# Performance work log

Hardware: AMD Instinct MI355X
Metric: run time of the kernel (lower is better)

## Reference

```python
import jax, jax.numpy as jnp
import numpy as np
import math

N_NODES = 50000
N_EDGES = 800000
IN_FEATS = 128
HID = 64
OUT = 2
D = 2  # num_layers


def calc_thetas(d):
    """Beta-distribution polynomial coefficients (ascending order), matching
    sympy.poly((x/2)**i * (1-x/2)**(d-i) / Beta(i+1, d+1-i)) with inverted coeffs."""
    thetas = []
    for i in range(d + 1):
        p1 = np.zeros(i + 1)
        p1[-1] = 0.5 ** i  # (x/2)^i, ascending coeffs
        p2 = np.array([math.comb(d - i, j) * (-0.5) ** j for j in range(d - i + 1)])  # (1-x/2)^(d-i)
        beta = math.factorial(i) * math.factorial(d - i) / math.factorial(d + 1)
        thetas.append((np.convolve(p1, p2) / beta).tolist())
    return thetas


def poly_branch(h, src, dst, thetas):
    """Run all PolyConv filters on activated features h; concat along feature dim."""
    n = h.shape[0]
    deg = jnp.zeros((n,), h.dtype).at[dst].add(jnp.ones((dst.shape[0],), h.dtype))
    dinv = jnp.clip(deg, 1.0, None) ** -0.5  # D^{-1/2} of in-degrees, clamped min 1
    dinv = dinv[:, None]
    outs = []
    for th in thetas:
        f = h
        acc = th[0] * h
        for k in range(1, len(th)):
            # feat <- feat - D^{-1/2} A D^{-1/2} feat  (copy_u / sum aggregation)
            agg = jax.ops.segment_sum((f * dinv)[src], dst, num_segments=n)
            f = f - agg * dinv
            acc = acc + th[k] * f
        outs.append(acc)
    return jnp.concatenate(outs, axis=-1)


def setup_inputs() -> dict:
    key = jax.random.key(0)
    ks = jax.random.split(key, 12)
    inp = {
        "x": jax.random.normal(ks[0], (N_NODES, IN_FEATS), jnp.float32),
        "sim_x": jax.random.normal(ks[1], (N_NODES, IN_FEATS), jnp.float32),
        "src": jax.random.randint(ks[2], (N_EDGES,), 0, N_NODES, jnp.int32),
        "dst": jax.random.randint(ks[3], (N_EDGES,), 0, N_NODES, jnp.int32),
        "sim_src": jax.random.randint(ks[4], (N_EDGES,), 0, N_NODES, jnp.int32),
        "sim_dst": jax.random.randint(ks[5], (N_EDGES,), 0, N_NODES, jnp.int32),
        "W1_o": jax.random.normal(ks[6], (IN_FEATS, HID), jnp.float32) / np.sqrt(IN_FEATS),
        "b1_o": jnp.zeros((HID,), jnp.float32),
        "W1_s": jax.random.normal(ks[7], (IN_FEATS, HID), jnp.float32) / np.sqrt(IN_FEATS),
        "b1_s": jnp.zeros((HID,), jnp.float32),
        "Wm1": jax.random.normal(ks[8], (HID * (D + 1) * 2, HID), jnp.float32) / np.sqrt(HID * (D + 1) * 2),
        "bm1": jnp.zeros((HID,), jnp.float32),
        "Wm2": jax.random.normal(ks[9], (HID, OUT), jnp.float32) / np.sqrt(HID),
        "bm2": jnp.zeros((OUT,), jnp.float32),
    }
    return inp


def reference(x, sim_x, src, dst, sim_src, sim_dst,
              W1_o, b1_o, W1_s, b1_s, Wm1, bm1, Wm2, bm2):
    thetas_o = calc_thetas(D)
    thetas_s = [[4.0] * (D + 1) for _ in range(D + 1)]  # conv_s uses constant theta=4

    h = jax.nn.relu(x @ W1_o + b1_o)
    h_final = poly_branch(h, src, dst, thetas_o)      # [N, HID*(D+1)]

    sh = jax.nn.relu(sim_x @ W1_s + b1_s)
    sim_h_final = poly_branch(sh, sim_src, sim_dst, thetas_s)

    h_all = jnp.concatenate([h_final, sim_h_final], axis=-1)  # [N, HID*(D+1)*2]
    logits = jax.nn.relu(h_all @ Wm1 + bm1) @ Wm2 + bm2
    return (h_all, logits)
```

## Files before the change

### kernel.cpp

```cpp
#include <hip/hip_runtime.h>
#include <hip/hip_fp16.h>
#include <hip/hip_fp8.h>


#define KB_BITS 10
#define KMAX 64
#define PCHUNK 4096
#define PVPT 16
#define PADMAX 7168

__device__ __forceinline__ float cv8(unsigned char b) {
    __hip_fp8_e4m3 v; v.__x = b; return (float)v;
}
__device__ __forceinline__ unsigned char to8(float f) {
    __hip_fp8_e4m3 v(f); return v.__x;
}

__global__ __launch_bounds__(256) void bhist_kernel(
    const int* __restrict__ dst, const int* __restrict__ sim_dst,
    int* __restrict__ bhist, int E, int Es) {
    __shared__ int h[2 * KMAX];
    int tid = threadIdx.x;
    if (tid < 2 * KMAX) h[tid] = 0;
    __syncthreads();
    int total = E + Es;
    for (int e = blockIdx.x * 256 + tid; e < total; e += gridDim.x * 256) {
        if (e < E) atomicAdd(&h[dst[e] >> KB_BITS], 1);
        else       atomicAdd(&h[KMAX + (sim_dst[e - E] >> KB_BITS)], 1);
    }
    __syncthreads();
    if (tid < 2 * KMAX && h[tid]) atomicAdd(&bhist[tid], h[tid]);
}

__global__ __launch_bounds__(128) void bscan_kernel(
    const int* __restrict__ bhist, int* __restrict__ brow,
    int* __restrict__ gcur) {
    int g = threadIdx.x >> 6, lane = threadIdx.x & 63;
    int v = bhist[g * KMAX + lane];
    int inc = v;
    #pragma unroll
    for (int off = 1; off < 64; off <<= 1) {
        int u = __shfl_up(inc, off);
        if (lane >= off) inc += u;
    }
    int ex = inc - v;
    brow[g * (KMAX + 1) + lane] = ex;
    if (lane == 63) brow[g * (KMAX + 1) + KMAX] = inc;
    gcur[g * KMAX + lane] = ex;
}

__global__ __launch_bounds__(256) void partition_kernel(
    const int* __restrict__ src, const int* __restrict__ dst,
    const int* __restrict__ sim_src, const int* __restrict__ sim_dst,
    int* __restrict__ gcur, unsigned* __restrict__ staged,
    int E, int Es, int nbo) {
    int b = blockIdx.x;
    const int* S; const int* D; int Eg; int goff; unsigned* stg;
    if (b < nbo) { S = src; D = dst; Eg = E; goff = 0; stg = staged; }
    else { b -= nbo; S = sim_src; D = sim_dst; Eg = Es; goff = KMAX; stg = staged + E; }
    int e0 = b * PCHUNK;
    int cnt_blk = Eg - e0; if (cnt_blk > PCHUNK) cnt_blk = PCHUNK;
    __shared__ int hist[KMAX], basep[KMAX], cur[KMAX], gbase[KMAX];
    __shared__ unsigned srt[PCHUNK];
    int tid = threadIdx.x;
    if (tid < KMAX) hist[tid] = 0;
    __syncthreads();
    unsigned full[PVPT];
    #pragma unroll
    for (int i = 0; i < PVPT; ++i) {
        int idx = i * 256 + tid;
        if (idx < cnt_blk) {
            int e = e0 + idx;
            int d = D[e];
            unsigned bk = (unsigned)d >> KB_BITS;
            full[i] = (bk << 26) | ((unsigned)S[e] << KB_BITS) |
                      (unsigned)(d & ((1 << KB_BITS) - 1));
            atomicAdd(&hist[bk], 1);
        } else full[i] = 0xFFFFFFFFu;
    }
    __syncthreads();
    if (tid < 64) {
        int v = hist[tid];
        int inc = v;
        #pragma unroll
        for (int off = 1; off < 64; off <<= 1) {
            int u = __shfl_up(inc, off);
            if (tid >= off) inc += u;
        }
        int ex = inc - v;
        basep[tid] = ex;
        cur[tid] = ex;
        gbase[tid] = v ? atomicAdd(&gcur[goff + tid], v) : 0;
    }
    __syncthreads();
    #pragma unroll
    for (int i = 0; i < PVPT; ++i) {
        unsigned f = full[i];
        if (f != 0xFFFFFFFFu) {
            unsigned bk = f >> 26;
            int slot = atomicAdd(&cur[bk], 1);
            srt[slot] = f;
        }
    }
    __syncthreads();
    for (int slot = tid; slot < cnt_blk; slot += 256) {
        unsigned f = srt[slot];
        unsigned bk = f >> 26;
        int gpos = gbase[bk] + (slot - basep[bk]);
        stg[gpos] = f & 0x3FFFFFFu;
    }
}

__global__ __launch_bounds__(512) void place_kernel(
    const unsigned* __restrict__ staged, const int* __restrict__ brow,
    int* __restrict__ row_o, int* __restrict__ row_s,
    int* __restrict__ pend_o, int* __restrict__ pend_s,
    unsigned short* __restrict__ esrc_o, unsigned short* __restrict__ esrc_s,
    float* __restrict__ dinv, int N, int K, int E, int pad) {
    int b = blockIdx.x;
    const unsigned* stg; const int* br; int* row; int* pend;
    unsigned short* esrc; float* dv;
    if (b < K) { stg = staged; br = brow; row = row_o; pend = pend_o; esrc = esrc_o; dv = dinv; }
    else { b -= K; stg = staged + E; br = brow + (KMAX + 1); row = row_s; pend = pend_s; esrc = esrc_s; dv = dinv + N; }
    int node0 = b << KB_BITS;
    int nn = N - node0; if (nn > (1 << KB_BITS)) nn = (1 << KB_BITS);
    int seg0 = br[b], seg1 = br[b + 1];
    int base = pad ? (seg0 + b * PADMAX) : seg0;
    __shared__ int ncnt[1 << KB_BITS];
    __shared__ int wsum[8];
    int tid = threadIdx.x;
    for (int i = tid; i < (1 << KB_BITS); i += 512) ncnt[i] = 0;
    __syncthreads();
    for (int j = seg0 + tid; j < seg1; j += 512)
        atomicAdd(&ncnt[stg[j] & ((1 << KB_BITS) - 1)], 1);
    __syncthreads();
    int i0 = tid * 2;
    int v0 = ncnt[i0], v1 = ncnt[i0 + 1];
    int p0 = pad ? ((v0 + 7) & ~7) : v0;
    int p1 = pad ? ((v1 + 7) & ~7) : v1;
    int s = p0 + p1;
    int inc = s;
    #pragma unroll
    for (int off = 1; off < 64; off <<= 1) {
        int u = __shfl_up(inc, off);
        if ((tid & 63) >= off) inc += u;
    }
    if ((tid & 63) == 63) wsum[tid >> 6] = inc;
    __syncthreads();
    int wo = 0;
    for (int w = 0; w < (tid >> 6); ++w) wo += wsum[w];
    int ex = base + wo + inc - s;
    if (i0 < nn) {
        row[node0 + i0] = ex;
        pend[node0 + i0] = ex + p0;
        dv[node0 + i0] = rsqrtf((float)(v0 > 1 ? v0 : 1));
        for (int q = ex + v0; q < ex + p0; ++q) esrc[q] = (unsigned short)N;
    }
    if (i0 + 1 < nn) {
        int ex2 = ex + p0;
        row[node0 + i0 + 1] = ex2;
        pend[node0 + i0 + 1] = ex2 + p1;
        dv[node0 + i0 + 1] = rsqrtf((float)(v1 > 1 ? v1 : 1));
        for (int q = ex2 + v1; q < ex2 + p1; ++q) esrc[q] = (unsigned short)N;
    }
    if (!pad && b == K - 1 && tid == 0) row[N] = br[K];
    __syncthreads();
    ncnt[i0] = ex;
    ncnt[i0 + 1] = ex + p0;
    __syncthreads();
    for (int j = seg0 + tid; j < seg1; j += 512) {
        unsigned f = stg[j];
        int pos = atomicAdd(&ncnt[f & ((1 << KB_BITS) - 1)], 1);
        esrc[pos] = (unsigned short)(f >> KB_BITS);
    }
}

__global__ __launch_bounds__(256) void fold_kernel(
    const float* __restrict__ Wm1, float* __restrict__ w1f,
    int* __restrict__ bhist) {
    int i = blockIdx.x * 256 + threadIdx.x;
    if (blockIdx.x == 0 && threadIdx.x < 2 * KMAX) bhist[threadIdx.x] = 0;
    if (i >= 256 * 64) return;
    int k = i >> 6, j = i & 63;
    float v = Wm1[k * 64 + j];
    if (k >= 192) v += Wm1[(k + 64) * 64 + j] + Wm1[(k + 128) * 64 + j];
    w1f[i] = v;
}

__global__ __launch_bounds__(256) void in_gemm2_kernel(
    const float* __restrict__ x, const float* __restrict__ sim_x,
    const float* __restrict__ W1_o, const float* __restrict__ b1_o,
    const float* __restrict__ W1_s, const float* __restrict__ b1_s,
    float* __restrict__ hall, __half* __restrict__ h16_o, __half* __restrict__ h16_s,
    __half* __restrict__ g16_o, __half* __restrict__ g16_s,
    unsigned char* __restrict__ h8_o, unsigned char* __restrict__ h8_s,
    unsigned char* __restrict__ g8_o, unsigned char* __restrict__ g8_s,
    const float* __restrict__ dinv, int n, int nbh, int f16path, int pad, int use8) {
    int bb = blockIdx.x;
    const float* xin; const float* W; const float* b; __half* h16;
    unsigned char* h8; const float* dinvv; int off;
    if (bb < nbh) { xin = x; W = W1_o; b = b1_o; h16 = h16_o; h8 = h8_o; dinvv = dinv; off = 0; }
    else { bb -= nbh; xin = sim_x; W = W1_s; b = b1_s; h16 = h16_s; h8 = h8_s; dinvv = dinv + n; off = 192; }
    if (pad && threadIdx.x < 64) {
        if (blockIdx.x == 0) {
            h16_o[(long)n * 64 + threadIdx.x] = __float2half_rn(0.f);
            g16_o[(long)n * 64 + threadIdx.x] = __float2half_rn(0.f);
            if (use8) { h8_o[(long)n * 64 + threadIdx.x] = 0; g8_o[(long)n * 64 + threadIdx.x] = 0; }
        } else if (blockIdx.x == nbh) {
            h16_s[(long)n * 64 + threadIdx.x] = __float2half_rn(0.f);
            g16_s[(long)n * 64 + threadIdx.x] = __float2half_rn(0.f);
            if (use8) { h8_s[(long)n * 64 + threadIdx.x] = 0; g8_s[(long)n * 64 + threadIdx.x] = 0; }
        }
    }
    __shared__ float xs[64][132];
    __shared__ float Wf[128][68];
    int tid = threadIdx.x;
    int node0 = bb * 64;
    const float4* wsrc = (const float4*)W;
    for (int i = tid; i < 2048; i += 256)
        *(float4*)&Wf[i >> 4][(i & 15) * 4] = wsrc[i];
    const float4* xsrc = (const float4*)xin;
    for (int i = tid; i < 2048; i += 256) {
        int nl = i >> 5, c = i & 31;
        int node = node0 + nl;
        float4 v = make_float4(0.f, 0.f, 0.f, 0.f);
        if (node < n) v = xsrc[(long)node * 32 + c];
        *(float4*)&xs[nl][c * 4] = v;
    }
    __syncthreads();
    int tx = tid & 15, ty = tid >> 4;
    float acc[4][4] = {};
    #pragma unroll 2
    for (int k = 0; k < 128; k += 4) {
        float4 a[4], bbv[4];
        #pragma unroll
        for (int i = 0; i < 4; ++i) a[i] = *(const float4*)&xs[ty * 4 + i][k];
        #pragma unroll
        for (int j = 0; j < 4; ++j) bbv[j] = *(const float4*)&Wf[k + j][tx * 4];
        #pragma unroll
        for (int i = 0; i < 4; ++i) {
            acc[i][0] = fmaf(a[i].x, bbv[0].x, acc[i][0]);
            acc[i][1] = fmaf(a[i].x, bbv[0].y, acc[i][1]);
            acc[i][2] = fmaf(a[i].x, bbv[0].z, acc[i][2]);
            acc[i][3] = fmaf(a[i].x, bbv[0].w, acc[i][3]);
            acc[i][0] = fmaf(a[i].y, bbv[1].x, acc[i][0]);
            acc[i][1] = fmaf(a[i].y, bbv[1].y, acc[i][1]);
            acc[i][2] = fmaf(a[i].y, bbv[1].z, acc[i][2]);
            acc[i][3] = fmaf(a[i].y, bbv[1].w, acc[i][3]);
            acc[i][0] = fmaf(a[i].z, bbv[2].x, acc[i][0]);
            acc[i][1] = fmaf(a[i].z, bbv[2].y, acc[i][1]);
            acc[i][2] = fmaf(a[i].z, bbv[2].z, acc[i][2]);
            acc[i][3] = fmaf(a[i].z, bbv[2].w, acc[i][3]);
            acc[i][0] = fmaf(a[i].w, bbv[3].x, acc[i][0]);
            acc[i][1] = fmaf(a[i].w, bbv[3].y, acc[i][1]);
            acc[i][2] = fmaf(a[i].w, bbv[3].z, acc[i][2]);
            acc[i][3] = fmaf(a[i].w, bbv[3].w, acc[i][3]);
        }
    }
    float4 bias = *(const float4*)&b[tx * 4];
    #pragma unroll
    for (int i = 0; i < 4; ++i) {
        int node = node0 + ty * 4 + i;
        if (node >= n) break;
        float4 r;
        r.x = fmaxf(acc[i][0] + bias.x, 0.0f);
        r.y = fmaxf(acc[i][1] + bias.y, 0.0f);
        r.z = fmaxf(acc[i][2] + bias.z, 0.0f);
        r.w = fmaxf(acc[i][3] + bias.w, 0.0f);
        if (f16path) {
            float dvn = dinvv[node];
            float v0 = r.x * dvn, v1 = r.y * dvn, v2 = r.z * dvn, v3 = r.w * dvn;
            __half hh[4];
            hh[0] = __float2half_rn(v0);
            hh[1] = __float2half_rn(v1);
            hh[2] = __float2half_rn(v2);
            hh[3] = __float2half_rn(v3);
            *(float2*)&h16[(long)node * 64 + tx * 4] = *(float2*)hh;
            if (use8) {
                uchar4 q;
                q.x = to8(v0); q.y = to8(v1); q.z = to8(v2); q.w = to8(v3);
                *(uchar4*)&h8[(long)node * 64 + tx * 4] = q;
            }
        } else {
            *(float4*)&hall[(long)node * 384 + off + tx * 4] = r;
        }
    }
}

__global__ __launch_bounds__(256) void hop1_kernel(
    const int* __restrict__ row_o, const int* __restrict__ pend_o,
    const unsigned short* __restrict__ esrc_o, const float* __restrict__ dinv_o,
    const int* __restrict__ row_s, const int* __restrict__ pend_s,
    const unsigned short* __restrict__ esrc_s, const float* __restrict__ dinv_s,
    const __half* __restrict__ h16_o, const __half* __restrict__ h16_s,
    __half* __restrict__ g16_o, __half* __restrict__ g16_s,
    const unsigned char* __restrict__ h8_o, const unsigned char* __restrict__ h8_s,
    unsigned char* __restrict__ g8_o, unsigned char* __restrict__ g8_s,
    int n, int nb, int use8) {
    int b = blockIdx.x;
    const int* row; const int* pend; const unsigned short* esrc;
    const float* dinv; const __half* h16; __half* g16;
    const unsigned char* h8; unsigned char* g8;
    if (b < nb) { row = row_o; pend = pend_o; esrc = esrc_o; dinv = dinv_o;
                  h16 = h16_o; g16 = g16_o; h8 = h8_o; g8 = g8_o; }
    else { b -= nb; row = row_s; pend = pend_s; esrc = esrc_s; dinv = dinv_s;
           h16 = h16_s; g16 = g16_s; h8 = h8_s; g8 = g8_s; }
    int d = b * 4 + (threadIdx.x >> 6);
    if (d >= n) return;
    int lane = threadIdx.x & 63;
    int p = row[d], end = pend[d];
    float dd = dinv[d];
    float h16v = __half2float(h16[((unsigned)d << 6) | lane]);
    float a0 = 0.f, a1 = 0.f, a2 = 0.f, a3 = 0.f;
    if (use8) {
        for (; p + 16 <= end; p += 16) {
            unsigned ss[16];
            #pragma unroll
            for (int i = 0; i < 16; ++i) ss[i] = esrc[p + i];
            #pragma unroll
            for (int i = 0; i < 16; i += 4) {
                a0 += cv8(h8[(ss[i] << 6) | lane]);
                a1 += cv8(h8[(ss[i + 1] << 6) | lane]);
                a2 += cv8(h8[(ss[i + 2] << 6) | lane]);
                a3 += cv8(h8[(ss[i + 3] << 6) | lane]);
            }
        }
        if (p + 8 <= end) {
            unsigned ss[8];
            #pragma unroll
            for (int i = 0; i < 8; ++i) ss[i] = esrc[p + i];
            #pragma unroll
            for (int i = 0; i < 8; i += 4) {
                a0 += cv8(h8[(ss[i] << 6) | lane]);
                a1 += cv8(h8[(ss[i + 1] << 6) | lane]);
                a2 += cv8(h8[(ss[i + 2] << 6) | lane]);
                a3 += cv8(h8[(ss[i + 3] << 6) | lane]);
            }
            p += 8;
        }
        for (; p < end; ++p)
            a0 += cv8(h8[((unsigned)esrc[p] << 6) | lane]);
    } else {
        for (; p + 16 <= end; p += 16) {
            unsigned ss[16];
            #pragma unroll
            for (int i = 0; i < 16; ++i) ss[i] = esrc[p + i];
            #pragma unroll
            for (int i = 0; i < 16; i += 4) {
                a0 += __half2float(h16[(ss[i] << 6) | lane]);
                a1 += __half2float(h16[(ss[i + 1] << 6) | lane]);
                a2 += __half2float(h16[(ss[i + 2] << 6) | lane]);
                a3 += __half2float(h16[(ss[i + 3] << 6) | lane]);
            }
        }
        if (p + 8 <= end) {
            unsigned ss[8];
            #pragma unroll
            for (int i = 0; i < 8; ++i) ss[i] = esrc[p + i];
            #pragma unroll
            for (int i = 0; i < 8; i += 4) {
                a0 += __half2float(h16[(ss[i] << 6) | lane]);
                a1 += __half2float(h16[(ss[i + 1] << 6) | lane]);
                a2 += __half2float(h16[(ss[i + 2] << 6) | lane]);
                a3 += __half2float(h16[(ss[i + 3] << 6) | lane]);
            }
            p += 8;
        }
        for (; p + 4 <= end; p += 4) {
            unsigned s0 = esrc[p], s1 = esrc[p + 1], s2 = esrc[p + 2], s3 = esrc[p + 3];
            a0 += __half2float(h16[(s0 << 6) | lane]);
            a1 += __half2float(h16[(s1 << 6) | lane]);
            a2 += __half2float(h16[(s2 << 6) | lane]);
            a3 += __half2float(h16[(s3 << 6) | lane]);
        }
        for (; p < end; ++p)
            a0 += __half2float(h16[((unsigned)esrc[p] << 6) | lane]);
    }
    float acc = (a0 + a1) + (a2 + a3);
    float val = h16v - acc * dd * dd;
    g16[((unsigned)d << 6) | lane] = __float2half_rn(val);
    if (use8) g8[((unsigned)d << 6) | lane] = to8(val);
}

__global__ __launch_bounds__(256) void hop2_kernel(
    const int* __restrict__ row_o, const int* __restrict__ pend_o,
    const unsigned short* __restrict__ esrc_o, const float* __restrict__ dinv_o,
    const int* __restrict__ row_s, const int* __restrict__ pend_s,
    const unsigned short* __restrict__ esrc_s, const float* __restrict__ dinv_s,
    const __half* __restrict__ h16_o, const __half* __restrict__ h16_s,
    const __half* __restrict__ g16_o, const __half* __restrict__ g16_s,
    const unsigned char* __restrict__ g8_o, const unsigned char* __restrict__ g8_s,
    float* __restrict__ hall, int n, int nb, int use8) {
    int b = blockIdx.x;
    int g = (b < nb) ? 0 : 1;
    const int* row; const int* pend; const unsigned short* esrc;
    const float* dinv; const __half* h16; const __half* g16;
    const unsigned char* g8;
    if (g == 0) { row = row_o; pend = pend_o; esrc = esrc_o; dinv = dinv_o;
                  h16 = h16_o; g16 = g16_o; g8 = g8_o; }
    else { b -= nb; row = row_s; pend = pend_s; esrc = esrc_s; dinv = dinv_s;
           h16 = h16_s; g16 = g16_s; g8 = g8_s; }
    int d = b * 4 + (threadIdx.x >> 6);
    if (d >= n) return;
    int lane = threadIdx.x & 63;
    int p = row[d], end = pend[d];
    float dd = dinv[d];
    float sq = 1.0f / dd;
    float f0 = __half2float(h16[((unsigned)d << 6) | lane]) * sq;
    float f1 = __half2float(g16[((unsigned)d << 6) | lane]) * sq;
    float a0 = 0.f, a1 = 0.f, a2 = 0.f, a3 = 0.f;
    if (use8) {
        for (; p + 16 <= end; p += 16) {
            unsigned ss[16];
            #pragma unroll
            for (int i = 0; i < 16; ++i) ss[i] = esrc[p + i];
            #pragma unroll
            for (int i = 0; i < 16; i += 4) {
                a0 += cv8(g8[(ss[i] << 6) | lane]);
                a1 += cv8(g8[(ss[i + 1] << 6) | lane]);
                a2 += cv8(g8[(ss[i + 2] << 6) | lane]);
                a3 += cv8(g8[(ss[i + 3] << 6) | lane]);
            }
        }
        if (p + 8 <= end) {
            unsigned ss[8];
            #pragma unroll
            for (int i = 0; i < 8; ++i) ss[i] = esrc[p + i];
            #pragma unroll
            for (int i = 0; i < 8; i += 4) {
                a0 += cv8(g8[(ss[i] << 6) | lane]);
                a1 += cv8(g8[(ss[i + 1] << 6) | lane]);
                a2 += cv8(g8[(ss[i + 2] << 6) | lane]);
                a3 += cv8(g8[(ss[i + 3] << 6) | lane]);
            }
            p += 8;
        }
        for (; p < end; ++p)
            a0 += cv8(g8[((unsigned)esrc[p] << 6) | lane]);
    } else {
        for (; p + 16 <= end; p += 16) {
            unsigned ss[16];
            #pragma unroll
            for (int i = 0; i < 16; ++i) ss[i] = esrc[p + i];
            #pragma unroll
            for (int i = 0; i < 16; i += 4) {
                a0 += __half2float(g16[(ss[i] << 6) | lane]);
                a1 += __half2float(g16[(ss[i + 1] << 6) | lane]);
                a2 += __half2float(g16[(ss[i + 2] << 6) | lane]);
                a3 += __half2float(g16[(ss[i + 3] << 6) | lane]);
            }
        }
        if (p + 8 <= end) {
            unsigned ss[8];
            #pragma unroll
            for (int i = 0; i < 8; ++i) ss[i] = esrc[p + i];
            #pragma unroll
            for (int i = 0; i < 8; i += 4) {
                a0 += __half2float(g16[(ss[i] << 6) | lane]);
                a1 += __half2float(g16[(ss[i + 1] << 6) | lane]);
                a2 += __half2float(g16[(ss[i + 2] << 6) | lane]);
                a3 += __half2float(g16[(ss[i + 3] << 6) | lane]);
            }
            p += 8;
        }
        for (; p + 4 <= end; p += 4) {
            unsigned s0 = esrc[p], s1 = esrc[p + 1], s2 = esrc[p + 2], s3 = esrc[p + 3];
            a0 += __half2float(g16[(s0 << 6) | lane]);
            a1 += __half2float(g16[(s1 << 6) | lane]);
            a2 += __half2float(g16[(s2 << 6) | lane]);
            a3 += __half2float(g16[(s3 << 6) | lane]);
        }
        for (; p < end; ++p)
            a0 += __half2float(g16[((unsigned)esrc[p] << 6) | lane]);
    }
    float acc = (a0 + a1) + (a2 + a3);
    float f2 = f1 - acc * dd;
    long ob = (long)d * 384 + lane;
    if (g == 0) {
        hall[ob]       = 3.0f * f0 - 3.0f * f1 + 0.75f * f2;
        hall[ob + 64]  = 3.0f * f1 - 1.5f * f2;
        hall[ob + 128] = 0.75f * f2;
    } else {
        float ss = 4.0f * (f0 + f1 + f2);
        hall[ob + 192] = ss; hall[ob + 256] = ss; hall[ob + 320] = ss;
    }
}

__global__ __launch_bounds__(256) void gather2_kernel(
    const int* __restrict__ row_o, const unsigned short* __restrict__ esrc_o,
    const float* __restrict__ dinv_o,
    const int* __restrict__ row_s, const unsigned short* __restrict__ esrc_s,
    const float* __restrict__ dinv_s,
    float* __restrict__ hall, int in_off_o, int in_off_s, int n, int nb) {
    int b = blockIdx.x;
    const int* row; const unsigned short* esrc; const float* dinv; int in_off;
    if (b < nb) { row = row_o; esrc = esrc_o; dinv = dinv_o; in_off = in_off_o; }
    else { b -= nb; row = row_s; esrc = esrc_s; dinv = dinv_s; in_off = in_off_s; }
    int d = b * 4 + (threadIdx.x >> 6);
    if (d >= n) return;
    int lane = threadIdx.x & 63;
    int p = row[d], end = row[d + 1];
    const float* fin = hall + in_off;
    float a0 = 0.f, a1 = 0.f, a2 = 0.f, a3 = 0.f;
    for (; p + 4 <= end; p += 4) {
        int s0 = esrc[p], s1 = esrc[p + 1], s2 = esrc[p + 2], s3 = esrc[p + 3];
        a0 = fmaf(fin[(long)s0 * 384 + lane], dinv[s0], a0);
        a1 = fmaf(fin[(long)s1 * 384 + lane], dinv[s1], a1);
        a2 = fmaf(fin[(long)s2 * 384 + lane], dinv[s2], a2);
        a3 = fmaf(fin[(long)s3 * 384 + lane], dinv[s3], a3);
    }
    for (; p < end; ++p) {
        int s = esrc[p];
        a0 = fmaf(fin[(long)s * 384 + lane], dinv[s], a0);
    }
    float acc = (a0 + a1) + (a2 + a3);
    long ob = (long)d * 384 + lane;
    hall[ob + in_off + 64] = fin[ob] - acc * dinv[d];
}

__global__ __launch_bounds__(256) void combine_kernel(float* __restrict__ h, int nf) {
    int i = blockIdx.x * 256 + threadIdx.x;
    if (i >= nf) return;
    long ob = (long)(i >> 6) * 384 + (i & 63);
    float f0v = h[ob], f1v = h[ob + 64], f2v = h[ob + 128];
    h[ob]       = 3.0f * f0v - 3.0f * f1v + 0.75f * f2v;
    h[ob + 64]  = 3.0f * f1v - 1.5f * f2v;
    h[ob + 128] = 0.75f * f2v;
    float ss = 4.0f * (h[ob + 192] + h[ob + 256] + h[ob + 320]);
    h[ob + 192] = ss; h[ob + 256] = ss; h[ob + 320] = ss;
}

__global__ __launch_bounds__(256) void mlp_kernel(
    const float* __restrict__ hall, const float* __restrict__ w1f,
    const float* __restrict__ bm1, const float* __restrict__ Wm2,
    const float* __restrict__ bm2, float* __restrict__ logits, int n) {
    __shared__ float xs[64][132];
    __shared__ float Wf[128][68];
    int tid = threadIdx.x;
    int node0 = blockIdx.x * 64;
    int tx = tid & 15, ty = tid >> 4;
    float acc[4][4] = {};
    const float4* wsrc = (const float4*)w1f;
    const float4* hsrc = (const float4*)hall;
    for (int c = 0; c < 2; ++c) {
        __syncthreads();
        for (int i = tid; i < 2048; i += 256)
            *(float4*)&Wf[i >> 4][(i & 15) * 4] = wsrc[c * 2048 + i];
        for (int i = tid; i < 2048; i += 256) {
            int nl = i >> 5, cc = i & 31;
            int node = node0 + nl;
            float4 v = make_float4(0.f, 0.f, 0.f, 0.f);
            if (node < n) v = hsrc[(long)node * 96 + c * 32 + cc];
            *(float4*)&xs[nl][cc * 4] = v;
        }
        __syncthreads();
        #pragma unroll 2
        for (int k = 0; k < 128; k += 4) {
            float4 a[4], bb[4];
            #pragma unroll
            for (int i = 0; i < 4; ++i) a[i] = *(const float4*)&xs[ty * 4 + i][k];
            #pragma unroll
            for (int j = 0; j < 4; ++j) bb[j] = *(const float4*)&Wf[k + j][tx * 4];
            #pragma unroll
            for (int i = 0; i < 4; ++i) {
                acc[i][0] = fmaf(a[i].x, bb[0].x, acc[i][0]);
                acc[i][1] = fmaf(a[i].x, bb[0].y, acc[i][1]);
                acc[i][2] = fmaf(a[i].x, bb[0].z, acc[i][2]);
                acc[i][3] = fmaf(a[i].x, bb[0].w, acc[i][3]);
                acc[i][0] = fmaf(a[i].y, bb[1].x, acc[i][0]);
                acc[i][1] = fmaf(a[i].y, bb[1].y, acc[i][1]);
                acc[i][2] = fmaf(a[i].y, bb[1].z, acc[i][2]);
                acc[i][3] = fmaf(a[i].y, bb[1].w, acc[i][3]);
                acc[i][0] = fmaf(a[i].z, bb[2].x, acc[i][0]);
                acc[i][1] = fmaf(a[i].z, bb[2].y, acc[i][1]);
                acc[i][2] = fmaf(a[i].z, bb[2].z, acc[i][2]);
                acc[i][3] = fmaf(a[i].z, bb[2].w, acc[i][3]);
                acc[i][0] = fmaf(a[i].w, bb[3].x, acc[i][0]);
                acc[i][1] = fmaf(a[i].w, bb[3].y, acc[i][1]);
                acc[i][2] = fmaf(a[i].w, bb[3].z, acc[i][2]);
                acc[i][3] = fmaf(a[i].w, bb[3].w, acc[i][3]);
            }
        }
    }
    __syncthreads();
    float4 bias = *(const float4*)&bm1[tx * 4];
    #pragma unroll
    for (int i = 0; i < 4; ++i) {
        xs[ty * 4 + i][tx * 4 + 0] = fmaxf(acc[i][0] + bias.x, 0.0f);
        xs[ty * 4 + i][tx * 4 + 1] = fmaxf(acc[i][1] + bias.y, 0.0f);
        xs[ty * 4 + i][tx * 4 + 2] = fmaxf(acc[i][2] + bias.z, 0.0f);
        xs[ty * 4 + i][tx * 4 + 3] = fmaxf(acc[i][3] + bias.w, 0.0f);
    }
    __syncthreads();
    if (tid < 128) {
        int nl = tid >> 1, o = tid & 1;
        int node = node0 + nl;
        if (node < n) {
            float p = bm2[o];
            #pragma unroll 8
            for (int k = 0; k < 64; ++k) p = fmaf(xs[nl][k], Wm2[k * 2 + o], p);
            logits[(long)node * 2 + o] = p;
        }
    }
}

extern "C" void kernel_launch(void* const* d_in, const int* in_sizes, int n_in,
                              void* d_out, int out_size, void* d_ws, size_t ws_size,
                              hipStream_t stream) {
    const float* x     = (const float*)d_in[0];
    const float* sim_x = (const float*)d_in[1];
    const int* src     = (const int*)d_in[2];
    const int* dst     = (const int*)d_in[3];
    const int* sim_src = (const int*)d_in[4];
    const int* sim_dst = (const int*)d_in[5];
    const float* W1_o = (const float*)d_in[6];
    const float* b1_o = (const float*)d_in[7];
    const float* W1_s = (const float*)d_in[8];
    const float* b1_s = (const float*)d_in[9];
    const float* Wm1  = (const float*)d_in[10];
    const float* bm1  = (const float*)d_in[11];
    const float* Wm2  = (const float*)d_in[12];
    const float* bm2  = (const float*)d_in[13];

    const int N  = in_sizes[0] / 128;
    const int E  = in_sizes[2];
    const int Es = in_sizes[4];
    const int NF = N * 64;
    const int K  = (N + (1 << KB_BITS) - 1) >> KB_BITS;

    float* hall = (float*)d_out;
    float* lgt  = hall + (long)N * 384;
    float* dinv = lgt;
    float* dinv_o = dinv;
    float* dinv_s = dinv + N;

    int* row_o  = (int*)d_ws;
    int* row_s  = row_o + (N + 1);
    int* pend_o = row_s + (N + 1);
    int* pend_s = pend_o + N;
    unsigned short* esrc_o = (unsigned short*)(pend_s + N);
    long esz_pad   = ((long)E + (long)K * PADMAX + 1) & ~1L;
    long esz_pad_s = ((long)Es + (long)K * PADMAX + 1) & ~1L;
    long esz_b     = ((long)E + 1) & ~1L;
    long esz_b_s   = ((long)Es + 1) & ~1L;

    unsigned short* esrc_sA = esrc_o + esz_pad;
    int* bhistA = (int*)(esrc_sA + esz_pad_s);
    unsigned short* esrc_sB = esrc_o + esz_b;
    int* bhistB = (int*)(esrc_sB + esz_b_s);

    auto layout_tail = [&](int* bh, bool with8) -> char* {
        int* br = bh + 2 * KMAX;
        int* gc = br + 2 * (KMAX + 1);
        float* wf = (float*)(gc + 2 * KMAX);
        __half* h = (__half*)(wf + 256 * 64);
        char* t = (char*)(h + 4 * (long)(N + 1) * 64);
        if (with8) t += 4 * (long)(N + 1) * 64;
        return t;
    };
    bool u16ok = N <= 65535;
    bool padA2 = u16ok && (size_t)(layout_tail(bhistA, true)  - (char*)d_ws) <= ws_size;
    bool padA  = padA2 ||
        (u16ok && (size_t)(layout_tail(bhistA, false) - (char*)d_ws) <= ws_size);
    unsigned short* esrc_s = padA ? esrc_sA : esrc_sB;
    int* bhist  = padA ? bhistA : bhistB;
    int* brow   = bhist + 2 * KMAX;
    int* gcur   = brow + 2 * (KMAX + 1);
    float* w1f  = (float*)(gcur + 2 * KMAX);
    __half* h16_o = (__half*)(w1f + 256 * 64);
    __half* h16_s = h16_o + (long)(N + 1) * 64;
    __half* g16_o = h16_s + (long)(N + 1) * 64;
    __half* g16_s = g16_o + (long)(N + 1) * 64;
    unsigned char* h8_o = (unsigned char*)(g16_s + (long)(N + 1) * 64);
    unsigned char* h8_s = h8_o + (long)(N + 1) * 64;
    unsigned char* g8_o = h8_s + (long)(N + 1) * 64;
    unsigned char* g8_s = g8_o + (long)(N + 1) * 64;
    bool f16path = u16ok && (padA ||
        ((size_t)(layout_tail(bhistB, false) - (char*)d_ws) <= ws_size));
    int pad = padA ? 1 : 0;
    int use8 = padA2 ? 1 : 0;
    unsigned* staged = (unsigned*)h16_o;
    const int* pend_o_use = pad ? pend_o : (row_o + 1);
    const int* pend_s_use = pad ? pend_s : (row_s + 1);

    int nb4  = (N + 3) / 4;
    int nb64 = (N + 63) / 64;
    int nfb  = (NF + 255) / 256;
    int nbo  = (E + PCHUNK - 1) / PCHUNK;
    int nbs  = (Es + PCHUNK - 1) / PCHUNK;

    fold_kernel<<<64, 256, 0, stream>>>(Wm1, w1f, bhist);
    bhist_kernel<<<256, 256, 0, stream>>>(dst, sim_dst, bhist, E, Es);
    bscan_kernel<<<1, 128, 0, stream>>>(bhist, brow, gcur);
    partition_kernel<<<nbo + nbs, 256, 0, stream>>>(src, dst, sim_src, sim_dst,
                                                    gcur, staged, E, Es, nbo);
    place_kernel<<<2 * K, 512, 0, stream>>>(staged, brow, row_o, row_s,
                                            pend_o, pend_s, esrc_o, esrc_s,
                                            dinv, N, K, E, pad);

    in_gemm2_kernel<<<2 * nb64, 256, 0, stream>>>(x, sim_x, W1_o, b1_o, W1_s, b1_s,
                                                  hall, h16_o, h16_s, g16_o, g16_s,
                                                  h8_o, h8_s, g8_o, g8_s,
                                                  dinv, N, nb64, f16path ? 1 : 0,
                                                  pad, use8);

    if (f16path) {
        hop1_kernel<<<2 * nb4, 256, 0, stream>>>(row_o, pend_o_use, esrc_o, dinv_o,
                                                 row_s, pend_s_use, esrc_s, dinv_s,
                                                 h16_o, h16_s, g16_o, g16_s,
                                                 h8_o, h8_s, g8_o, g8_s,
                                                 N, nb4, use8);
        hop2_kernel<<<2 * nb4, 256, 0, stream>>>(row_o, pend_o_use, esrc_o, dinv_o,
                                                 row_s, pend_s_use, esrc_s, dinv_s,
                                                 h16_o, h16_s, g16_o, g16_s,
                                                 g8_o, g8_s, hall, N, nb4, use8);
    } else {
        gather2_kernel<<<2 * nb4, 256, 0, stream>>>(row_o, esrc_o, dinv_o,
                                                    row_s, esrc_s, dinv_s,
                                                    hall, 0, 192, N, nb4);
        gather2_kernel<<<2 * nb4, 256, 0, stream>>>(row_o, esrc_o, dinv_o,
                                                    row_s, esrc_s, dinv_s,
                                                    hall, 64, 256, N, nb4);
        combine_kernel<<<nfb, 256, 0, stream>>>(hall, NF);
    }

    mlp_kernel<<<nb64, 256, 0, stream>>>(hall, w1f, bm1, Wm2, bm2, lgt, N);
}
```

Measured before the change: 351.5 us.

## Store GEMM tiles as fp16 in LDS, double rows per block, shuffle-reduce logits

Both the input GEMM and the MLP GEMM now convert their operands to half precision when staging them in shared memory. This cuts LDS footprint and bandwidth, and lets each block cover 128 nodes instead of 64, with 8 rows per thread instead of 4. The MLP's second layer now reduces the per-thread partial logits with wavefront xor-shuffles instead of writing hidden activations to shared memory and running a serial dot product in half the threads. Rounding inputs and weights to fp16 loses accuracy, and the larger per-thread tile raises register pressure and halves the number of blocks.

```diff
diff --git a/kernel.cpp b/kernel.cpp
--- a/kernel.cpp
+++ b/kernel.cpp
@@ -212,69 +212,70 @@
             if (use8) { h8_s[(long)n * 64 + threadIdx.x] = 0; g8_s[(long)n * 64 + threadIdx.x] = 0; }
         }
     }
-    __shared__ float xs[64][132];
-    __shared__ float Wf[128][68];
+    __shared__ __half xh[128][132];
+    __shared__ __half Wfh[128][68];
     int tid = threadIdx.x;
-    int node0 = bb * 64;
+    int node0 = bb * 128;
     const float4* wsrc = (const float4*)W;
-    for (int i = tid; i < 2048; i += 256)
-        *(float4*)&Wf[i >> 4][(i & 15) * 4] = wsrc[i];
+    for (int i = tid; i < 2048; i += 256) {
+        float4 w = wsrc[i];
+        __half hh[4];
+        hh[0] = __float2half_rn(w.x); hh[1] = __float2half_rn(w.y);
+        hh[2] = __float2half_rn(w.z); hh[3] = __float2half_rn(w.w);
+        *(float2*)&Wfh[i >> 4][(i & 15) * 4] = *(float2*)hh;
+    }
     const float4* xsrc = (const float4*)xin;
-    for (int i = tid; i < 2048; i += 256) {
+    for (int i = tid; i < 4096; i += 256) {
         int nl = i >> 5, c = i & 31;
         int node = node0 + nl;
         float4 v = make_float4(0.f, 0.f, 0.f, 0.f);
         if (node < n) v = xsrc[(long)node * 32 + c];
-        *(float4*)&xs[nl][c * 4] = v;
+        __half hh[4];
+        hh[0] = __float2half_rn(v.x); hh[1] = __float2half_rn(v.y);
+        hh[2] = __float2half_rn(v.z); hh[3] = __float2half_rn(v.w);
+        *(float2*)&xh[nl][c * 4] = *(float2*)hh;
     }
     __syncthreads();
     int tx = tid & 15, ty = tid >> 4;
-    float acc[4][4] = {};
-    #pragma unroll 2
+    float acc[8][4] = {};
     for (int k = 0; k < 128; k += 4) {
-        float4 a[4], bbv[4];
+        float bf[4][4];
         #pragma unroll
-        for (int i = 0; i < 4; ++i) a[i] = *(const float4*)&xs[ty * 4 + i][k];
+        for (int j = 0; j < 4; ++j) {
+            float2 raw = *(const float2*)&Wfh[k + j][tx * 4];
+            __half2* hp = (__half2*)&raw;
+            float2 lo = __half22float2(hp[0]), hi = __half22float2(hp[1]);
+            bf[j][0] = lo.x; bf[j][1] = lo.y; bf[j][2] = hi.x; bf[j][3] = hi.y;
+        }
         #pragma unroll
-        for (int j = 0; j < 4; ++j) bbv[j] = *(const float4*)&Wf[k + j][tx * 4];
-        #pragma unroll
-        for (int i = 0; i < 4; ++i) {
-            acc[i][0] = fmaf(a[i].x, bbv[0].x, acc[i][0]);
-            acc[i][1] = fmaf(a[i].x, bbv[0].y, acc[i][1]);
-            acc[i][2] = fmaf(a[i].x, bbv[0].z, acc[i][2]);
-            acc[i][3] = fmaf(a[i].x, bbv[0].w, acc[i][3]);
-            acc[i][0] = fmaf(a[i].y, bbv[1].x, acc[i][0]);
-            acc[i][1] = fmaf(a[i].y, bbv[1].y, acc[i][1]);
-            acc[i][2] = fmaf(a[i].y, bbv[1].z, acc[i][2]);
-            acc[i][3] = fmaf(a[i].y, bbv[1].w, acc[i][3]);
-            acc[i][0] = fmaf(a[i].z, bbv[2].x, acc[i][0]);
-            acc[i][1] = fmaf(a[i].z, bbv[2].y, acc[i][1]);
-            acc[i][2] = fmaf(a[i].z, bbv[2].z, acc[i][2]);
-            acc[i][3] = fmaf(a[i].z, bbv[2].w, acc[i][3]);
-            acc[i][0] = fmaf(a[i].w, bbv[3].x, acc[i][0]);
-            acc[i][1] = fmaf(a[i].w, bbv[3].y, acc[i][1]);
-            acc[i][2] = fmaf(a[i].w, bbv[3].z, acc[i][2]);
-            acc[i][3] = fmaf(a[i].w, bbv[3].w, acc[i][3]);
+        for (int i = 0; i < 8; ++i) {
+            float2 raw = *(const float2*)&xh[ty * 8 + i][k];
+            __half2* hp = (__half2*)&raw;
+            float2 lo = __half22float2(hp[0]), hi = __half22float2(hp[1]);
+            #pragma unroll
+            for (int j2 = 0; j2 < 4; ++j2) {
+                acc[i][j2] = fmaf(lo.x, bf[0][j2], acc[i][j2]);
+                acc[i][j2] = fmaf(lo.y, bf[1][j2], acc[i][j2]);
+                acc[i][j2] = fmaf(hi.x, bf[2][j2], acc[i][j2]);
+                acc[i][j2] = fmaf(hi.y, bf[3][j2], acc[i][j2]);
+            }
         }
     }
     float4 bias = *(const float4*)&b[tx * 4];
     #pragma unroll
-    for (int i = 0; i < 4; ++i) {
-        int node = node0 + ty * 4 + i;
+    for (int i = 0; i < 8; ++i) {
+        int node = node0 + ty * 8 + i;
         if (node >= n) break;
-        float4 r;
-        r.x = fmaxf(acc[i][0] + bias.x, 0.0f);
-        r.y = fmaxf(acc[i][1] + bias.y, 0.0f);
-        r.z = fmaxf(acc[i][2] + bias.z, 0.0f);
-        r.w = fmaxf(acc[i][3] + bias.w, 0.0f);
+        float r0 = fmaxf(acc[i][0] + bias.x, 0.0f);
+        float r1 = fmaxf(acc[i][1] + bias.y, 0.0f);
+        float r2 = fmaxf(acc[i][2] + bias.z, 0.0f);
+        float r3 = fmaxf(acc[i][3] + bias.w, 0.0f);
         if (f16path) {
             float dvn = dinvv[node];
-            float v0 = r.x * dvn, v1 = r.y * dvn, v2 = r.z * dvn, v3 = r.w * dvn;
+            float v0 = r0 * dvn, v1 = r1 * dvn, v2 = r2 * dvn, v3 = r3 * dvn;
             __half hh[4];
-            hh[0] = __float2half_rn(v0);
-            hh[1] = __float2half_rn(v1);
-            hh[2] = __float2half_rn(v2);
-            hh[3] = __float2half_rn(v3);
+            hh[0] = __float2half_rn(v0); hh[1] = __float2half_rn(v1);
+            hh[2] = __float2half_rn(v2); hh[3] = __float2half_rn(v3);
             *(float2*)&h16[(long)node * 64 + tx * 4] = *(float2*)hh;
             if (use8) {
                 uchar4 q;
@@ -282,6 +283,7 @@
                 *(uchar4*)&h8[(long)node * 64 + tx * 4] = q;
             }
         } else {
+            float4 r; r.x = r0; r.y = r1; r.z = r2; r.w = r3;
             *(float4*)&hall[(long)node * 384 + off + tx * 4] = r;
         }
     }
@@ -534,72 +536,83 @@
     const float* __restrict__ hall, const float* __restrict__ w1f,
     const float* __restrict__ bm1, const float* __restrict__ Wm2,
     const float* __restrict__ bm2, float* __restrict__ logits, int n) {
-    __shared__ float xs[64][132];
-    __shared__ float Wf[128][68];
+    __shared__ __half xh[128][132];
+    __shared__ __half Wfh[128][68];
     int tid = threadIdx.x;
-    int node0 = blockIdx.x * 64;
+    int node0 = blockIdx.x * 128;
     int tx = tid & 15, ty = tid >> 4;
-    float acc[4][4] = {};
+    float acc[8][4] = {};
     const float4* wsrc = (const float4*)w1f;
     const float4* hsrc = (const float4*)hall;
     for (int c = 0; c < 2; ++c) {
         __syncthreads();
-        for (int i = tid; i < 2048; i += 256)
-            *(float4*)&Wf[i >> 4][(i & 15) * 4] = wsrc[c * 2048 + i];
         for (int i = tid; i < 2048; i += 256) {
+            float4 w = wsrc[c * 2048 + i];
+            __half hh[4];
+            hh[0] = __float2half_rn(w.x); hh[1] = __float2half_rn(w.y);
+            hh[2] = __float2half_rn(w.z); hh[3] = __float2half_rn(w.w);
+            *(float2*)&Wfh[i >> 4][(i & 15) * 4] = *(float2*)hh;
+        }
+        for (int i = tid; i < 4096; i += 256) {
             int nl = i >> 5, cc = i & 31;
             int node = node0 + nl;
             float4 v = make_float4(0.f, 0.f, 0.f, 0.f);
             if (node < n) v = hsrc[(long)node * 96 + c * 32 + cc];
-            *(float4*)&xs[nl][cc * 4] = v;
+            __half hh[4];
+            hh[0] = __float2half_rn(v.x); hh[1] = __float2half_rn(v.y);
+            hh[2] = __float2half_rn(v.z); hh[3] = __float2half_rn(v.w);
+            *(float2*)&xh[nl][cc * 4] = *(float2*)hh;
         }
         __syncthreads();
-        #pragma unroll 2
         for (int k = 0; k < 128; k += 4) {
-            float4 a[4], bb[4];
-            #pragma unroll
-            for (int i = 0; i < 4; ++i) a[i] = *(const float4*)&xs[ty * 4 + i][k];
-            #pragma unroll
-            for (int j = 0; j < 4; ++j) bb[j] = *(const float4*)&Wf[k + j][tx * 4];
-            #pragma unroll
-            for (int i = 0; i < 4; ++i) {
-                acc[i][0] = fmaf(a[i].x, bb[0].x, acc[i][0]);
-                acc[i][1] = fmaf(a[i].x, bb[0].y, acc[i][1]);
-                acc[i][2] = fmaf(a[i].x, bb[0].z, acc[i][2]);
-                acc[i][3] = fmaf(a[i].x, bb[0].w, acc[i][3]);
-                acc[i][0] = fmaf(a[i].y, bb[1].x, acc[i][0]);
-                acc[i][1] = fmaf(a[i].y, bb[1].y, acc[i][1]);
-                acc[i][2] = fmaf(a[i].y, bb[1].z, acc[i][2]);
-                acc[i][3] = fmaf(a[i].y, bb[1].w, acc[i][3]);
-                acc[i][0] = fmaf(a[i].z, bb[2].x, acc[i][0]);
-                acc[i][1] = fmaf(a[i].z, bb[2].y, acc[i][1]);
-                acc[i][2] = fmaf(a[i].z, bb[2].z, acc[i][2]);
-                acc[i][3] = fmaf(a[i].z, bb[2].w, acc[i][3]);
-                acc[i][0] = fmaf(a[i].w, bb[3].x, acc[i][0]);
-                acc[i][1] = fmaf(a[i].w, bb[3].y, acc[i][1]);
-                acc[i][2] = fmaf(a[i].w, bb[3].z, acc[i][2]);
-                acc[i][3] = fmaf(a[i].w, bb[3].w, acc[i][3]);
-            }
-        }
-    }
-    __syncthreads();
+            float bf[4][4];
+            #pragma unroll
+            for (int j = 0; j < 4; ++j) {
+                float2 raw = *(const float2*)&Wfh[k + j][tx * 4];
+                __half2* hp = (__half2*)&raw;
+                float2 lo = __half22float2(hp[0]), hi = __half22float2(hp[1]);
+                bf[j][0] = lo.x; bf[j][1] = lo.y; bf[j][2] = hi.x; bf[j][3] = hi.y;
+            }
+            #pragma unroll
+            for (int i = 0; i < 8; ++i) {
+                float2 raw = *(const float2*)&xh[ty * 8 + i][k];
+                __half2* hp = (__half2*)&raw;
+                float2 lo = __half22float2(hp[0]), hi = __half22float2(hp[1]);
+                #pragma unroll
+                for (int j2 = 0; j2 < 4; ++j2) {
+                    acc[i][j2] = fmaf(lo.x, bf[0][j2], acc[i][j2]);
+                    acc[i][j2] = fmaf(lo.y, bf[1][j2], acc[i][j2]);
+                    acc[i][j2] = fmaf(hi.x, bf[2][j2], acc[i][j2]);
+                    acc[i][j2] = fmaf(hi.y, bf[3][j2], acc[i][j2]);
+                }
+            }
+        }
+    }
     float4 bias = *(const float4*)&bm1[tx * 4];
+    float w2[4][2];
     #pragma unroll
-    for (int i = 0; i < 4; ++i) {
-        xs[ty * 4 + i][tx * 4 + 0] = fmaxf(acc[i][0] + bias.x, 0.0f);
-        xs[ty * 4 + i][tx * 4 + 1] = fmaxf(acc[i][1] + bias.y, 0.0f);
-        xs[ty * 4 + i][tx * 4 + 2] = fmaxf(acc[i][2] + bias.z, 0.0f);
-        xs[ty * 4 + i][tx * 4 + 3] = fmaxf(acc[i][3] + bias.w, 0.0f);
-    }
-    __syncthreads();
-    if (tid < 128) {
-        int nl = tid >> 1, o = tid & 1;
-        int node = node0 + nl;
-        if (node < n) {
-            float p = bm2[o];
-            #pragma unroll 8
-            for (int k = 0; k < 64; ++k) p = fmaf(xs[nl][k], Wm2[k * 2 + o], p);
-            logits[(long)node * 2 + o] = p;
+    for (int j = 0; j < 4; ++j) {
+        w2[j][0] = Wm2[(tx * 4 + j) * 2];
+        w2[j][1] = Wm2[(tx * 4 + j) * 2 + 1];
+    }
+    float bb0 = bm2[0], bb1 = bm2[1];
+    #pragma unroll
+    for (int i = 0; i < 8; ++i) {
+        float h0 = fmaxf(acc[i][0] + bias.x, 0.0f);
+        float h1 = fmaxf(acc[i][1] + bias.y, 0.0f);
+        float h2 = fmaxf(acc[i][2] + bias.z, 0.0f);
+        float h3 = fmaxf(acc[i][3] + bias.w, 0.0f);
+        float p0 = h0 * w2[0][0] + h1 * w2[1][0] + h2 * w2[2][0] + h3 * w2[3][0];
+        float p1 = h0 * w2[0][1] + h1 * w2[1][1] + h2 * w2[2][1] + h3 * w2[3][1];
+        #pragma unroll
+        for (int off = 1; off < 16; off <<= 1) {
+            p0 += __shfl_xor(p0, off);
+            p1 += __shfl_xor(p1, off);
+        }
+        int node = node0 + ty * 8 + i;
+        if (tx == 0 && node < n) {
+            logits[(long)node * 2]     = p0 + bb0;
+            logits[(long)node * 2 + 1] = p1 + bb1;
         }
     }
 }
@@ -683,11 +696,11 @@
     const int* pend_o_use = pad ? pend_o : (row_o + 1);
     const int* pend_s_use = pad ? pend_s : (row_s + 1);
 
-    int nb4  = (N + 3) / 4;
-    int nb64 = (N + 63) / 64;
-    int nfb  = (NF + 255) / 256;
-    int nbo  = (E + PCHUNK - 1) / PCHUNK;
-    int nbs  = (Es + PCHUNK - 1) / PCHUNK;
+    int nb4   = (N + 3) / 4;
+    int nb128 = (N + 127) / 128;
+    int nfb   = (NF + 255) / 256;
+    int nbo   = (E + PCHUNK - 1) / PCHUNK;
+    int nbs   = (Es + PCHUNK - 1) / PCHUNK;
 
     fold_kernel<<<64, 256, 0, stream>>>(Wm1, w1f, bhist);
     bhist_kernel<<<256, 256, 0, stream>>>(dst, sim_dst, bhist, E, Es);
@@ -698,11 +711,11 @@
                                             pend_o, pend_s, esrc_o, esrc_s,
                                             dinv, N, K, E, pad);
 
-    in_gemm2_kernel<<<2 * nb64, 256, 0, stream>>>(x, sim_x, W1_o, b1_o, W1_s, b1_s,
-                                                  hall, h16_o, h16_s, g16_o, g16_s,
-                                                  h8_o, h8_s, g8_o, g8_s,
-                                                  dinv, N, nb64, f16path ? 1 : 0,
-                                                  pad, use8);
+    in_gemm2_kernel<<<2 * nb128, 256, 0, stream>>>(x, sim_x, W1_o, b1_o, W1_s, b1_s,
+                                                   hall, h16_o, h16_s, g16_o, g16_s,
+                                                   h8_o, h8_s, g8_o, g8_s,
+                                                   dinv, N, nb128, f16path ? 1 : 0,
+                                                   pad, use8);
 
     if (f16path) {
         hop1_kernel<<<2 * nb4, 256, 0, stream>>>(row_o, pend_o_use, esrc_o, dinv_o,
@@ -724,5 +737,5 @@
         combine_kernel<<<nfb, 256, 0, stream>>>(hall, NF);
     }
 
-    mlp_kernel<<<nb64, 256, 0, stream>>>(hall, w1f, bm1, Wm2, bm2, lgt, N);
-}
+    mlp_kernel<<<nb128, 256, 0, stream>>>(hall, w1f, bm1, Wm2, bm2, lgt, N);
+}
```

New measurement: 358.0 us. About the same (+1.9%).
